# Optimization experiments

Measured on AMD Instinct MI355X. Metric: run time of the kernel, lower is better.

The kernel has to match this reference:

```python
import jax, jax.numpy as jnp
import numpy as np

TGT, BSZ, E = 256, 8, 256
SRC = 4096
H = 8
HD = E // H


def setup_inputs() -> dict:
    key = jax.random.key(0)
    ks = jax.random.split(key, 6)
    return {
        "query": jax.random.normal(ks[0], (TGT, BSZ, E), dtype=jnp.float32),
        "key": jax.random.normal(ks[1], (SRC, BSZ, E), dtype=jnp.float32),
        "value": jax.random.normal(ks[2], (SRC, BSZ, E), dtype=jnp.float32),
        "proposal_mask": jax.random.uniform(ks[3], (BSZ, TGT, SRC), dtype=jnp.float32),
        "out_proj_weight": jax.random.normal(ks[4], (E, E), dtype=jnp.float32) * (1.0 / np.sqrt(E)),
        "out_proj_bias": jax.random.normal(ks[5], (E,), dtype=jnp.float32) * 0.01,
    }


def reference(query, key, value, proposal_mask, out_proj_weight, out_proj_bias):
    tgt_len, bsz, embed_dim = query.shape
    src_len = key.shape[0]
    num_heads = H
    head_dim = embed_dim // num_heads

    # v: (src, bsz, E) -> (src, bsz*H, hd) -> (bsz*H, src, hd); index q = b*H + h
    v = value.reshape(src_len, bsz * num_heads, head_dim).transpose(1, 0, 2)

    # proposal_mask (bsz, tgt, src); torch loop+stack produces mask_nhead[b*H+h] = proposal_mask[b]
    mask_nhead = jnp.repeat(proposal_mask, num_heads, axis=0)  # (bsz*H, tgt, src)

    # weighted sum of values per head (no score compute)
    attn_output = jnp.einsum('qts,qsc->qtc', mask_nhead, v)  # (bsz*H, tgt, hd)

    # (bsz*H, tgt, hd) -> (tgt, bsz*H, hd) -> (tgt, bsz, E)
    attn_output = attn_output.transpose(1, 0, 2).reshape(tgt_len, bsz, embed_dim)

    # out projection (outDecoderLayer=False)
    attn_output = attn_output @ out_proj_weight.T + out_proj_bias

    # averaged weights: mask repeated per head -> mean over heads == proposal_mask
    attn_weights = mask_nhead.reshape(bsz, num_heads, tgt_len, src_len).sum(axis=1) / num_heads
    return attn_output, attn_weights
```

## Files before the change

### kernel.cpp

```cpp
#include <hip/hip_runtime.h>
#include <hip/hip_bf16.h>

#define TGT 256
#define BSZ 8
#define E   256
#define SRC 4096

typedef __attribute__((ext_vector_type(8))) short           bf16x8;
typedef __attribute__((ext_vector_type(4))) float           f32x4;
typedef __attribute__((ext_vector_type(4))) float           f4;
typedef __attribute__((ext_vector_type(8))) unsigned short  u16x8;

__device__ inline unsigned short f2b(float x) {
    union { __hip_bfloat16 h; unsigned short u; } cv;
    cv.h = __float2bfloat16(x);
    return cv.u;
}

__device__ inline bf16x8 cvt8v(const float* __restrict__ p) {
    f4 lo = *(const f4*)p;
    f4 hi = *(const f4*)(p + 4);
    bf16x8 r;
    #pragma unroll
    for (int j = 0; j < 4; ++j) { r[j] = (short)f2b(lo[j]); r[4 + j] = (short)f2b(hi[j]); }
    return r;
}

__global__ __launch_bounds__(256) void prep(
    const float* __restrict__ value, const float* __restrict__ wgt,
    const float* __restrict__ bias,
    unsigned short* __restrict__ vtf, unsigned short* __restrict__ wf,
    float* __restrict__ out0)
{
    const int tid = threadIdx.x;

    if (blockIdx.y == 9) {
        #pragma unroll
        for (int s = 0; s < 8; ++s) {
            int f4i = s * 16384 + blockIdx.x * 256 + tid;
            *(f4*)(out0 + (size_t)f4i * 4) = *(const f4*)(bias + (f4i & 63) * 4);
        }
        return;
    }

    if (blockIdx.y == 8) {
        if (tid < 128) {
            int o    = blockIdx.x * 128 + tid;
            int et   = o >> 9;
            int ks   = (o >> 6) & 7;
            int lane = o & 63;
            int quad = lane >> 4, l15 = lane & 15;
            bf16x8 v = cvt8v(wgt + (size_t)(et * 16 + l15) * E + ks * 32 + quad * 8);
            *(bf16x8*)&wf[(size_t)o * 8] = v;
        }
        return;
    }

    __shared__ unsigned short tile[64 * 264];
    const int kch = blockIdx.x;
    const int b   = blockIdx.y;
    const int k0  = kch * 64;

    #pragma unroll
    for (int i = 0; i < 16; ++i) {
        int lin = i * 256 + tid;
        int row = lin >> 6;
        int c4  = lin & 63;
        f4 v = *(const f4*)(value + (size_t)(k0 + row) * (BSZ * E)
                                  + (size_t)b * E + c4 * 4);
        #pragma unroll
        for (int j = 0; j < 4; ++j) tile[row * 264 + c4 * 4 + j] = f2b(v[j]);
    }
    __syncthreads();

    #pragma unroll
    for (int i = 0; i < 8; ++i) {
        int o    = i * 256 + tid;
        int et   = o >> 7;
        int ksl  = (o >> 6) & 1;
        int lane = o & 63;
        int quad = lane >> 4, l15 = lane & 15;
        u16x8 pk;
        #pragma unroll
        for (int j = 0; j < 8; ++j)
            pk[j] = tile[(ksl * 32 + quad * 8 + j) * 264 + et * 16 + l15];
        size_t ks = (size_t)kch * 2 + ksl;
        *(u16x8*)&vtf[((((size_t)b * 16 + et) * 128 + ks) * 64 + lane) * 8] = pk;
    }
}

#define AP 136
#define CP 264

__global__ __launch_bounds__(512) void gemm1(
    const float* __restrict__ mask,
    const unsigned short* __restrict__ vtf,
    const unsigned short* __restrict__ wf,
    float* __restrict__ out1,
    float* __restrict__ out0)
{
    __shared__ unsigned short As[2][32 * AP];
    const int bx  = blockIdx.x;
    const int b   = bx & 7;
    const int tt  = (bx >> 3) & 7;
    const int kc  = bx >> 6;
    const int t0  = tt * 32;
    const int k0  = kc * 512;
    const int tid = threadIdx.x;
    const int w    = tid >> 6;
    const int lane = tid & 63;
    const int quad = lane >> 4;
    const int l15  = lane & 15;

    const float* mbase = mask + (size_t)b * TGT * SRC + (size_t)t0 * SRC + k0;
    float*       obase = out1 + (size_t)b * TGT * SRC + (size_t)t0 * SRC + k0;
    const int sr0 = tid >> 5, sr1 = sr0 + 16, sc = (tid & 31) * 4;

    const unsigned short* bfr0 = vtf + (((size_t)b * 16 + 2 * w) * 128 + (size_t)kc * 16) * 512;
    const unsigned short* bfr1 = bfr0 + (size_t)128 * 512;

    {
        f4 v0 = *(const f4*)(mbase + (size_t)sr0 * SRC + sc);
        f4 v1 = *(const f4*)(mbase + (size_t)sr1 * SRC + sc);
        *(f4*)(obase + (size_t)sr0 * SRC + sc) = v0;
        *(f4*)(obase + (size_t)sr1 * SRC + sc) = v1;
        unsigned short* d0 = &As[0][sr0 * AP + sc];
        unsigned short* d1 = &As[0][sr1 * AP + sc];
        #pragma unroll
        for (int j = 0; j < 4; ++j) { d0[j] = f2b(v0[j]); d1[j] = f2b(v1[j]); }
    }
    __syncthreads();

    f32x4 acc00 = {}, acc01 = {}, acc10 = {}, acc11 = {};

    #pragma unroll
    for (int s = 0; s < 4; ++s) {
        f4 a0v, a1v;
        if (s < 3) {
            a0v = *(const f4*)(mbase + (size_t)sr0 * SRC + (s + 1) * 128 + sc);
            a1v = *(const f4*)(mbase + (size_t)sr1 * SRC + (s + 1) * 128 + sc);
        }
        #pragma unroll
        for (int q = 0; q < 4; ++q) {
            bf16x8 B0 = *(const bf16x8*)(bfr0 + ((size_t)(s * 4 + q) * 64 + lane) * 8);
            bf16x8 B1 = *(const bf16x8*)(bfr1 + ((size_t)(s * 4 + q) * 64 + lane) * 8);
            bf16x8 a0 = *(const bf16x8*)&As[s & 1][ l15       * AP + q * 32 + quad * 8];
            bf16x8 a1 = *(const bf16x8*)&As[s & 1][(l15 + 16) * AP + q * 32 + quad * 8];
            acc00 = __builtin_amdgcn_mfma_f32_16x16x32_bf16(a0, B0, acc00, 0, 0, 0);
            acc01 = __builtin_amdgcn_mfma_f32_16x16x32_bf16(a0, B1, acc01, 0, 0, 0);
            acc10 = __builtin_amdgcn_mfma_f32_16x16x32_bf16(a1, B0, acc10, 0, 0, 0);
            acc11 = __builtin_amdgcn_mfma_f32_16x16x32_bf16(a1, B1, acc11, 0, 0, 0);
        }
        if (s < 3) {
            *(f4*)(obase + (size_t)sr0 * SRC + (s + 1) * 128 + sc) = a0v;
            *(f4*)(obase + (size_t)sr1 * SRC + (s + 1) * 128 + sc) = a1v;
            unsigned short* d0 = &As[(s + 1) & 1][sr0 * AP + sc];
            unsigned short* d1 = &As[(s + 1) & 1][sr1 * AP + sc];
            #pragma unroll
            for (int j = 0; j < 4; ++j) { d0[j] = f2b(a0v[j]); d1[j] = f2b(a1v[j]); }
        }
        __syncthreads();
    }

    unsigned short* ct = &As[0][0];
    {
        const int c0 = w * 32 + l15;
        #pragma unroll
        for (int r = 0; r < 4; ++r) {
            int r0 = quad * 4 + r;
            ct[ r0       * CP + c0     ] = f2b(acc00[r]);
            ct[ r0       * CP + c0 + 16] = f2b(acc01[r]);
            ct[(r0 + 16) * CP + c0     ] = f2b(acc10[r]);
            ct[(r0 + 16) * CP + c0 + 16] = f2b(acc11[r]);
        }
    }
    __syncthreads();

    {
        const int et0 = 2 * w;
        const unsigned short* bf0 = wf + ((size_t)et0 * 8 * 64 + lane) * 8;
        const unsigned short* bf1 = bf0 + (size_t)8 * 64 * 8;
        f32x4 p00 = {}, p01 = {}, p10 = {}, p11 = {};
        #pragma unroll
        for (int ks = 0; ks < 8; ++ks) {
            bf16x8 aLo = *(const bf16x8*)&ct[ l15       * CP + ks * 32 + quad * 8];
            bf16x8 aHi = *(const bf16x8*)&ct[(l15 + 16) * CP + ks * 32 + quad * 8];
            bf16x8 b0  = *(const bf16x8*)(bf0 + (size_t)ks * 512);
            bf16x8 b1  = *(const bf16x8*)(bf1 + (size_t)ks * 512);
            p00 = __builtin_amdgcn_mfma_f32_16x16x32_bf16(aLo, b0, p00, 0, 0, 0);
            p01 = __builtin_amdgcn_mfma_f32_16x16x32_bf16(aLo, b1, p01, 0, 0, 0);
            p10 = __builtin_amdgcn_mfma_f32_16x16x32_bf16(aHi, b0, p10, 0, 0, 0);
            p11 = __builtin_amdgcn_mfma_f32_16x16x32_bf16(aHi, b1, p11, 0, 0, 0);
        }
        #pragma unroll
        for (int r = 0; r < 4; ++r) {
            int tA = t0 + quad * 4 + r;
            int tB = tA + 16;
            int eA = et0 * 16 + l15;
            float* oA = out0 + (size_t)tA * (BSZ * E) + (size_t)b * E;
            float* oB = out0 + (size_t)tB * (BSZ * E) + (size_t)b * E;
            atomicAdd(oA + eA,      p00[r]);
            atomicAdd(oA + eA + 16, p01[r]);
            atomicAdd(oB + eA,      p10[r]);
            atomicAdd(oB + eA + 16, p11[r]);
        }
    }
}

extern "C" void kernel_launch(void* const* d_in, const int* in_sizes, int n_in,
                              void* d_out, int out_size, void* d_ws, size_t ws_size,
                              hipStream_t stream)
{
    const float* value = (const float*)d_in[2];
    const float* mask  = (const float*)d_in[3];
    const float* wgt   = (const float*)d_in[4];
    const float* bias  = (const float*)d_in[5];

    float* out0 = (float*)d_out;
    float* out1 = (float*)d_out + (size_t)TGT * BSZ * E;

    unsigned short* vtf  = (unsigned short*)d_ws;
    unsigned short* wf   = vtf + (size_t)BSZ * E * SRC;

    prep<<<dim3(64, 10), 256, 0, stream>>>(value, wgt, bias, vtf, wf, out0);
    gemm1<<<512, 512, 0, stream>>>(mask, vtf, wf, out1, out0);
}
```

Baseline: 150.4 us.

## Fold output projection into value before mask GEMM (reassociate matmuls)

Reassociates (mask·V)·Wᵀ as mask·(V·Wᵀ), so the prep kernel projects the value tensor by the out-proj weight with MFMA before it is laid out in fragment order. The main GEMM then adds its accumulators straight into the output with atomics, which removes the per-block LDS round trip and the second MFMA projection stage. Shared-memory bf16 stores are also packed into 4-wide vector writes. The cost is an extra projection GEMM over the full value tensor in prep, where each wave reads and converts the fp32 weight from global memory. The projected values are also rounded to bf16 at a different point, which changes numerics slightly.

After: 210.9 us. +40.2%, slower.

```diff
diff --git a/kernel.cpp b/kernel.cpp
--- a/kernel.cpp
+++ b/kernel.cpp
@@ -10,6 +10,7 @@
 typedef __attribute__((ext_vector_type(4))) float           f32x4;
 typedef __attribute__((ext_vector_type(4))) float           f4;
 typedef __attribute__((ext_vector_type(8))) unsigned short  u16x8;
+typedef __attribute__((ext_vector_type(4))) unsigned short  u16x4;
 
 __device__ inline unsigned short f2b(float x) {
     union { __hip_bfloat16 h; unsigned short u; } cv;
@@ -26,15 +27,14 @@
     return r;
 }
 
-__global__ __launch_bounds__(256) void prep(
+__global__ __launch_bounds__(256) void prep_vw(
     const float* __restrict__ value, const float* __restrict__ wgt,
     const float* __restrict__ bias,
-    unsigned short* __restrict__ vtf, unsigned short* __restrict__ wf,
-    float* __restrict__ out0)
+    unsigned short* __restrict__ vwf, float* __restrict__ out0)
 {
     const int tid = threadIdx.x;
 
-    if (blockIdx.y == 9) {
+    if (blockIdx.y == 8) {
         #pragma unroll
         for (int s = 0; s < 8; ++s) {
             int f4i = s * 16384 + blockIdx.x * 256 + tid;
@@ -43,33 +43,47 @@
         return;
     }
 
-    if (blockIdx.y == 8) {
-        if (tid < 128) {
-            int o    = blockIdx.x * 128 + tid;
-            int et   = o >> 9;
-            int ks   = (o >> 6) & 7;
-            int lane = o & 63;
-            int quad = lane >> 4, l15 = lane & 15;
-            bf16x8 v = cvt8v(wgt + (size_t)(et * 16 + l15) * E + ks * 32 + quad * 8);
-            *(bf16x8*)&wf[(size_t)o * 8] = v;
-        }
-        return;
-    }
-
     __shared__ unsigned short tile[64 * 264];
-    const int kch = blockIdx.x;
-    const int b   = blockIdx.y;
-    const int k0  = kch * 64;
+    const int sc64 = blockIdx.x;
+    const int b    = blockIdx.y;
+    const int s0   = sc64 * 64;
 
     #pragma unroll
     for (int i = 0; i < 16; ++i) {
         int lin = i * 256 + tid;
         int row = lin >> 6;
         int c4  = lin & 63;
-        f4 v = *(const f4*)(value + (size_t)(k0 + row) * (BSZ * E)
+        f4 v = *(const f4*)(value + (size_t)(s0 + row) * (BSZ * E)
                                   + (size_t)b * E + c4 * 4);
-        #pragma unroll
-        for (int j = 0; j < 4; ++j) tile[row * 264 + c4 * 4 + j] = f2b(v[j]);
+        u16x4 pk;
+        #pragma unroll
+        for (int j = 0; j < 4; ++j) pk[j] = f2b(v[j]);
+        *(u16x4*)&tile[row * 264 + c4 * 4] = pk;
+    }
+    __syncthreads();
+
+    const int w    = tid >> 6;
+    const int lane = tid & 63;
+    const int quad = lane >> 4;
+    const int l15  = lane & 15;
+
+    bf16x8 a[8];
+    #pragma unroll
+    for (int ks = 0; ks < 8; ++ks)
+        a[ks] = *(const bf16x8*)&tile[(w * 16 + l15) * 264 + ks * 32 + quad * 8];
+
+    const float* wrow = wgt + (size_t)l15 * E + quad * 8;
+    #pragma unroll
+    for (int et = 0; et < 16; ++et) {
+        f32x4 acc = {};
+        #pragma unroll
+        for (int ks = 0; ks < 8; ++ks) {
+            bf16x8 bb = cvt8v(wrow + (size_t)(et * 16) * E + ks * 32);
+            acc = __builtin_amdgcn_mfma_f32_16x16x32_bf16(a[ks], bb, acc, 0, 0, 0);
+        }
+        #pragma unroll
+        for (int r = 0; r < 4; ++r)
+            tile[(w * 16 + quad * 4 + r) * 264 + et * 16 + l15] = f2b(acc[r]);
     }
     __syncthreads();
 
@@ -78,24 +92,22 @@
         int o    = i * 256 + tid;
         int et   = o >> 7;
         int ksl  = (o >> 6) & 1;
-        int lane = o & 63;
-        int quad = lane >> 4, l15 = lane & 15;
+        int ln   = o & 63;
+        int q2   = ln >> 4, p15 = ln & 15;
         u16x8 pk;
         #pragma unroll
         for (int j = 0; j < 8; ++j)
-            pk[j] = tile[(ksl * 32 + quad * 8 + j) * 264 + et * 16 + l15];
-        size_t ks = (size_t)kch * 2 + ksl;
-        *(u16x8*)&vtf[((((size_t)b * 16 + et) * 128 + ks) * 64 + lane) * 8] = pk;
+            pk[j] = tile[(ksl * 32 + q2 * 8 + j) * 264 + et * 16 + p15];
+        size_t ks = (size_t)sc64 * 2 + ksl;
+        *(u16x8*)&vwf[((((size_t)b * 16 + et) * 128 + ks) * 64 + ln) * 8] = pk;
     }
 }
 
 #define AP 136
-#define CP 264
 
 __global__ __launch_bounds__(512) void gemm1(
     const float* __restrict__ mask,
-    const unsigned short* __restrict__ vtf,
-    const unsigned short* __restrict__ wf,
+    const unsigned short* __restrict__ vwf,
     float* __restrict__ out1,
     float* __restrict__ out0)
 {
@@ -116,7 +128,7 @@
     float*       obase = out1 + (size_t)b * TGT * SRC + (size_t)t0 * SRC + k0;
     const int sr0 = tid >> 5, sr1 = sr0 + 16, sc = (tid & 31) * 4;
 
-    const unsigned short* bfr0 = vtf + (((size_t)b * 16 + 2 * w) * 128 + (size_t)kc * 16) * 512;
+    const unsigned short* bfr0 = vwf + (((size_t)b * 16 + 2 * w) * 128 + (size_t)kc * 16) * 512;
     const unsigned short* bfr1 = bfr0 + (size_t)128 * 512;
 
     {
@@ -124,10 +136,11 @@
         f4 v1 = *(const f4*)(mbase + (size_t)sr1 * SRC + sc);
         *(f4*)(obase + (size_t)sr0 * SRC + sc) = v0;
         *(f4*)(obase + (size_t)sr1 * SRC + sc) = v1;
-        unsigned short* d0 = &As[0][sr0 * AP + sc];
-        unsigned short* d1 = &As[0][sr1 * AP + sc];
-        #pragma unroll
-        for (int j = 0; j < 4; ++j) { d0[j] = f2b(v0[j]); d1[j] = f2b(v1[j]); }
+        u16x4 p0, p1;
+        #pragma unroll
+        for (int j = 0; j < 4; ++j) { p0[j] = f2b(v0[j]); p1[j] = f2b(v1[j]); }
+        *(u16x4*)&As[0][sr0 * AP + sc] = p0;
+        *(u16x4*)&As[0][sr1 * AP + sc] = p1;
     }
     __syncthreads();
 
@@ -154,55 +167,27 @@
         if (s < 3) {
             *(f4*)(obase + (size_t)sr0 * SRC + (s + 1) * 128 + sc) = a0v;
             *(f4*)(obase + (size_t)sr1 * SRC + (s + 1) * 128 + sc) = a1v;
-            unsigned short* d0 = &As[(s + 1) & 1][sr0 * AP + sc];
-            unsigned short* d1 = &As[(s + 1) & 1][sr1 * AP + sc];
+            u16x4 p0, p1;
             #pragma unroll
-            for (int j = 0; j < 4; ++j) { d0[j] = f2b(a0v[j]); d1[j] = f2b(a1v[j]); }
+            for (int j = 0; j < 4; ++j) { p0[j] = f2b(a0v[j]); p1[j] = f2b(a1v[j]); }
+            *(u16x4*)&As[(s + 1) & 1][sr0 * AP + sc] = p0;
+            *(u16x4*)&As[(s + 1) & 1][sr1 * AP + sc] = p1;
         }
         __syncthreads();
     }
 
-    unsigned short* ct = &As[0][0];
     {
         const int c0 = w * 32 + l15;
-        #pragma unroll
-        for (int r = 0; r < 4; ++r) {
-            int r0 = quad * 4 + r;
-            ct[ r0       * CP + c0     ] = f2b(acc00[r]);
-            ct[ r0       * CP + c0 + 16] = f2b(acc01[r]);
-            ct[(r0 + 16) * CP + c0     ] = f2b(acc10[r]);
-            ct[(r0 + 16) * CP + c0 + 16] = f2b(acc11[r]);
-        }
-    }
-    __syncthreads();
-
-    {
-        const int et0 = 2 * w;
-        const unsigned short* bf0 = wf + ((size_t)et0 * 8 * 64 + lane) * 8;
-        const unsigned short* bf1 = bf0 + (size_t)8 * 64 * 8;
-        f32x4 p00 = {}, p01 = {}, p10 = {}, p11 = {};
-        #pragma unroll
-        for (int ks = 0; ks < 8; ++ks) {
-            bf16x8 aLo = *(const bf16x8*)&ct[ l15       * CP + ks * 32 + quad * 8];
-            bf16x8 aHi = *(const bf16x8*)&ct[(l15 + 16) * CP + ks * 32 + quad * 8];
-            bf16x8 b0  = *(const bf16x8*)(bf0 + (size_t)ks * 512);
-            bf16x8 b1  = *(const bf16x8*)(bf1 + (size_t)ks * 512);
-            p00 = __builtin_amdgcn_mfma_f32_16x16x32_bf16(aLo, b0, p00, 0, 0, 0);
-            p01 = __builtin_amdgcn_mfma_f32_16x16x32_bf16(aLo, b1, p01, 0, 0, 0);
-            p10 = __builtin_amdgcn_mfma_f32_16x16x32_bf16(aHi, b0, p10, 0, 0, 0);
-            p11 = __builtin_amdgcn_mfma_f32_16x16x32_bf16(aHi, b1, p11, 0, 0, 0);
-        }
         #pragma unroll
         for (int r = 0; r < 4; ++r) {
             int tA = t0 + quad * 4 + r;
             int tB = tA + 16;
-            int eA = et0 * 16 + l15;
             float* oA = out0 + (size_t)tA * (BSZ * E) + (size_t)b * E;
             float* oB = out0 + (size_t)tB * (BSZ * E) + (size_t)b * E;
-            atomicAdd(oA + eA,      p00[r]);
-            atomicAdd(oA + eA + 16, p01[r]);
-            atomicAdd(oB + eA,      p10[r]);
-            atomicAdd(oB + eA + 16, p11[r]);
+            atomicAdd(oA + c0,      acc00[r]);
+            atomicAdd(oA + c0 + 16, acc01[r]);
+            atomicAdd(oB + c0,      acc10[r]);
+            atomicAdd(oB + c0 + 16, acc11[r]);
         }
     }
 }
@@ -219,9 +204,8 @@
     float* out0 = (float*)d_out;
     float* out1 = (float*)d_out + (size_t)TGT * BSZ * E;
 
-    unsigned short* vtf  = (unsigned short*)d_ws;
-    unsigned short* wf   = vtf + (size_t)BSZ * E * SRC;
-
-    prep<<<dim3(64, 10), 256, 0, stream>>>(value, wgt, bias, vtf, wf, out0);
-    gemm1<<<512, 512, 0, stream>>>(mask, vtf, wf, out1, out0);
-}
+    unsigned short* vwf = (unsigned short*)d_ws;
+
+    prep_vw<<<dim3(64, 9), 256, 0, stream>>>(value, wgt, bias, vwf, out0);
+    gemm1<<<512, 512, 0, stream>>>(mask, vwf, out1, out0);
+}
```
